# Kernel optimization log

Measured on AMD Instinct MI355X. Metric: run time of the kernel, lower is better.

The kernel has to match this reference:

```python
import jax, jax.numpy as jnp
import numpy as np

CH = 256
GROUPS = 8
EPS = 1e-5


def setup_inputs() -> dict:
    key = jax.random.key(0)
    ks = jax.random.split(key, 12)
    b, c, h, w = 8, CH, 64, 64
    s = 0.02
    return {
        "x": jax.random.normal(ks[0], (b, c, h, w), dtype=jnp.float32),
        "gn_w": jnp.ones((c,), dtype=jnp.float32),
        "gn_b": jnp.zeros((c,), dtype=jnp.float32),
        "wq": jax.random.normal(ks[1], (c, c), dtype=jnp.float32) * s,
        "bq": jax.random.normal(ks[2], (c,), dtype=jnp.float32) * s,
        "wk": jax.random.normal(ks[3], (c, c), dtype=jnp.float32) * s,
        "bk": jax.random.normal(ks[4], (c,), dtype=jnp.float32) * s,
        "wv": jax.random.normal(ks[5], (c, c), dtype=jnp.float32) * s,
        "bv": jax.random.normal(ks[6], (c,), dtype=jnp.float32) * s,
        "wp": jax.random.normal(ks[7], (c, c), dtype=jnp.float32) * s,
        "bp": jax.random.normal(ks[8], (c,), dtype=jnp.float32) * s,
    }


def reference(x, gn_w, gn_b, wq, bq, wk, bk, wv, bv, wp, bp):
    b, c, h, w = x.shape
    n = h * w
    # GroupNorm(8, c): normalize over (c//g, h, w) per group, then affine per-channel
    xg = x.reshape(b, GROUPS, c // GROUPS, n)
    mu = xg.mean(axis=(2, 3), keepdims=True)
    var = xg.var(axis=(2, 3), keepdims=True)
    y = ((xg - mu) * jax.lax.rsqrt(var + EPS)).reshape(b, c, n)
    y = y * gn_w[None, :, None] + gn_b[None, :, None]
    # 1x1 convs == channel matmuls
    q = jnp.einsum('oc,bcn->bno', wq, y) + bq              # [b, n, c]
    k = jnp.einsum('oc,bcn->bon', wk, y) + bk[:, None]     # [b, c, n]
    v = jnp.einsum('oc,bcn->bno', wv, y) + bv              # [b, n, c]
    scale = 1.0 / jnp.sqrt(jnp.float32(c))
    attn = jax.nn.softmax(jnp.einsum('bnc,bcm->bnm', q, k) * scale, axis=-1)  # [b, n, n]
    out = jnp.einsum('bnm,bmc->bcn', attn, v)              # [b, c, n]
    proj = jnp.einsum('oc,bcn->bon', wp, out) + bp[:, None]
    return x + proj.reshape(b, c, h, w)
```

## Files before the change

kernel.cpp:

```cpp
#include <hip/hip_runtime.h>

typedef __attribute__((ext_vector_type(8))) short s16x8;
typedef __attribute__((ext_vector_type(4))) float f32x4;
typedef __attribute__((ext_vector_type(16))) float f32x16;
typedef __attribute__((ext_vector_type(4))) uint u32x4;
typedef __attribute__((ext_vector_type(2))) uint u32x2;
typedef __attribute__((ext_vector_type(2))) long s64x2;
typedef __attribute__((ext_vector_type(8))) int i32x8;
typedef unsigned char u8;

#define MFMA16(a, b, c) __builtin_amdgcn_mfma_f32_16x16x32_bf16((a), (b), (c), 0, 0, 0)
#define MFMAF8(a, b, c) __builtin_amdgcn_mfma_f32_32x32x16_fp8_fp8((a), (b), (c), 0, 0, 0)
#define MFMAMX(a, b, c) \
  __builtin_amdgcn_mfma_scale_f32_32x32x64_f8f6f4((a), (b), (c), 0, 0, 0, 0x7F7F7F7F, 0, 0x7F7F7F7F)

__device__ __forceinline__ ushort f2bf(float f) {
  uint u = __builtin_bit_cast(uint, f);
  u = (u + 0x7fffu + ((u >> 16) & 1u)) >> 16;
  return (ushort)u;
}
__device__ __forceinline__ float max3f(float a, float b, float c) {
  return fmaxf(fmaxf(a, b), c);
}

__global__ __launch_bounds__(256) void cvt_w_kernel(
    const float* __restrict__ s0, const float* __restrict__ s1,
    const float* __restrict__ s2, const float* __restrict__ s3,
    ushort* __restrict__ d0, ushort* __restrict__ d1,
    ushort* __restrict__ d2, ushort* __restrict__ d3,
    const float* __restrict__ bq, const float* __restrict__ bk,
    const float* __restrict__ bv, float* __restrict__ bcat) {
  int i = blockIdx.x * 256 + threadIdx.x;
  const float4* s[4] = {(const float4*)s0, (const float4*)s1, (const float4*)s2, (const float4*)s3};
  ushort* d[4] = {d0, d1, d2, d3};
#pragma unroll
  for (int m = 0; m < 4; ++m) {
    float4 v = s[m][i];
    uint lo = (uint)f2bf(v.x) | ((uint)f2bf(v.y) << 16);
    uint hi = (uint)f2bf(v.z) | ((uint)f2bf(v.w) << 16);
    *(uint2*)(d[m] + (size_t)i * 4) = make_uint2(lo, hi);
  }
  if (blockIdx.x == 0) {
    int t = threadIdx.x;
    bcat[t] = bq[t];
    bcat[256 + t] = bk[t];
    bcat[512 + t] = bv[t];
  }
}

__global__ __launch_bounds__(256) void gn_stats_kernel(
    const float* __restrict__ x, float2* __restrict__ partial) {
  int bid = blockIdx.x;
  int b = bid >> 6, g = (bid >> 3) & 7, sl = bid & 7;
  const float4* src = (const float4*)(x + ((size_t)b * 256 + g * 32) * 4096) + sl * 4096;
  float s = 0.f, ss = 0.f;
#pragma unroll 4
  for (int i = threadIdx.x; i < 4096; i += 256) {
    float4 v = src[i];
    s += v.x + v.y + v.z + v.w;
    ss += v.x * v.x + v.y * v.y + v.z * v.z + v.w * v.w;
  }
#pragma unroll
  for (int off = 32; off; off >>= 1) {
    s += __shfl_down(s, off);
    ss += __shfl_down(ss, off);
  }
  __shared__ float ps[4], pss[4];
  int w = threadIdx.x >> 6, lane = threadIdx.x & 63;
  if (lane == 0) { ps[w] = s; pss[w] = ss; }
  __syncthreads();
  if (threadIdx.x == 0) {
    float2 r;
    r.x = ps[0] + ps[1] + ps[2] + ps[3];
    r.y = pss[0] + pss[1] + pss[2] + pss[3];
    partial[bid] = r;
  }
}

__global__ __launch_bounds__(256) void gn_apply_kernel(
    const float* __restrict__ x, const float2* __restrict__ partial,
    const float* __restrict__ gw, const float* __restrict__ gb,
    ushort* __restrict__ y) {
  int bid = blockIdx.x;
  int b = bid >> 8;
  int rem = bid & 255;
  int ct = rem >> 6, nt = rem & 63;
  int t = threadIdx.x;
  __shared__ float xs[64][65];
  __shared__ float smu2[2], srs2[2];
  if (t < 2) {
    float S = 0.f, SS = 0.f;
#pragma unroll
    for (int i = 0; i < 8; ++i) {
      float2 p = partial[(b << 6) | ((2 * ct + t) << 3) | i];
      S += p.x;
      SS += p.y;
    }
    float mu = S * (1.f / 131072.f);
    float var = SS * (1.f / 131072.f) - mu * mu;
    smu2[t] = mu;
    srs2[t] = rsqrtf(var + 1e-5f);
  }
  const float* xb = x + ((size_t)b * 256 + ct * 64) * 4096 + nt * 64;
  {
    int r = t >> 2, q = t & 3;
    const float4* src = (const float4*)(xb + (size_t)r * 4096 + q * 16);
#pragma unroll
    for (int i = 0; i < 4; ++i) {
      float4 v = src[i];
      xs[r][q * 16 + i * 4 + 0] = v.x;
      xs[r][q * 16 + i * 4 + 1] = v.y;
      xs[r][q * 16 + i * 4 + 2] = v.z;
      xs[r][q * 16 + i * 4 + 3] = v.w;
    }
  }
  __syncthreads();
  {
    int nr = t >> 2, q = t & 3;
    int c0 = q * 16;
    ushort tmp[16];
#pragma unroll
    for (int i = 0; i < 16; ++i) {
      int ci = c0 + i;
      int ch = ct * 64 + ci;
      int gsel = ci >> 5;
      float sc = gw[ch] * srs2[gsel];
      float sh = gb[ch] - smu2[gsel] * sc;
      float v = xs[ci][nr] * sc + sh;
      tmp[i] = f2bf(v);
    }
    ushort* dst = y + ((size_t)b * 4096 + nt * 64 + nr) * 256 + ct * 64 + c0;
    uint p[8];
#pragma unroll
    for (int j = 0; j < 8; ++j) p[j] = (uint)tmp[2 * j] | ((uint)tmp[2 * j + 1] << 16);
    *(uint4*)dst = make_uint4(p[0], p[1], p[2], p[3]);
    *((uint4*)dst + 1) = make_uint4(p[4], p[5], p[6], p[7]);
  }
}

template <int MODE>
__global__ __launch_bounds__(256) void gemm_bt(
    const ushort* __restrict__ A, const ushort* __restrict__ B,
    size_t aB, size_t bB, int M, int N,
    const float* __restrict__ bias, const float* __restrict__ resid,
    size_t rB, void* __restrict__ Cout, size_t cB) {
  int mTiles = M >> 7;
  int tm = blockIdx.x % mTiles, tn = blockIdx.x / mTiles;
  const ushort* Ab = A + blockIdx.y * aB + (size_t)tm * 128 * 256;
  const ushort* Bb = B + blockIdx.y * bB + (size_t)tn * 128 * 256;

  __shared__ ushort As[2][8192];
  __shared__ ushort Bs[2][8192];

  int t = threadIdx.x, lane = t & 63, w = t >> 6;
  int wr = w >> 1, wc = w & 1, lq = lane & 15, lg = lane >> 4;

  f32x4 acc[4][4];
#pragma unroll
  for (int i = 0; i < 4; ++i)
#pragma unroll
    for (int j = 0; j < 4; ++j) acc[i][j] = f32x4{0.f, 0.f, 0.f, 0.f};

  auto stageT = [&](int kb, int db) {
#pragma unroll
    for (int i = 0; i < 4; ++i) {
      int bu = i * 256 + w * 64;
      int u = bu + lane;
      int row = u >> 3, c = u & 7;
      int cl = c ^ (row & 7);
      const ushort* sa = Ab + (size_t)row * 256 + kb * 64 + cl * 8;
      __builtin_amdgcn_global_load_lds(
          (const __attribute__((address_space(1))) uint*)sa,
          (__attribute__((address_space(3))) uint*)(&As[db][0] + bu * 8), 16, 0, 0);
      const ushort* sb = Bb + (size_t)row * 256 + kb * 64 + cl * 8;
      __builtin_amdgcn_global_load_lds(
          (const __attribute__((address_space(1))) uint*)sb,
          (__attribute__((address_space(3))) uint*)(&Bs[db][0] + bu * 8), 16, 0, 0);
    }
  };

  stageT(0, 0);

#pragma unroll 1
  for (int kb = 0; kb < 4; ++kb) {
    if (kb < 3) {
      stageT(kb + 1, (kb + 1) & 1);
      asm volatile("s_waitcnt vmcnt(8)" ::: "memory");
    } else {
      asm volatile("s_waitcnt vmcnt(0)" ::: "memory");
    }
    __builtin_amdgcn_s_barrier();
    const ushort* Abf = &As[kb & 1][0];
    const ushort* Bbf = &Bs[kb & 1][0];
#pragma unroll
    for (int ks = 0; ks < 2; ++ks) {
      s16x8 af[4], bf[4];
#pragma unroll
      for (int mt = 0; mt < 4; ++mt) {
        int row = wr * 64 + mt * 16 + lq;
        af[mt] = *(const s16x8*)&Abf[row * 64 + (((ks * 4 + lg) ^ (row & 7)) << 3)];
      }
#pragma unroll
      for (int nt = 0; nt < 4; ++nt) {
        int row = wc * 64 + nt * 16 + lq;
        bf[nt] = *(const s16x8*)&Bbf[row * 64 + (((ks * 4 + lg) ^ (row & 7)) << 3)];
      }
#pragma unroll
      for (int mt = 0; mt < 4; ++mt)
#pragma unroll
        for (int nt = 0; nt < 4; ++nt)
          acc[mt][nt] = MFMA16(af[mt], bf[nt], acc[mt][nt]);
    }
    asm volatile("" ::: "memory");
    __builtin_amdgcn_s_barrier();
    asm volatile("" ::: "memory");
  }

  int mBase = tm * 128 + wr * 64;
  int nBase = tn * 128 + wc * 64;
#pragma unroll
  for (int mt = 0; mt < 4; ++mt) {
#pragma unroll
    for (int nt = 0; nt < 4; ++nt) {
#pragma unroll
      for (int r = 0; r < 4; ++r) {
        int row = mBase + mt * 16 + lg * 4 + r;
        int col = nBase + nt * 16 + lq;
        float v = acc[mt][nt][r];
        if (MODE == 6) {
          v += bias[col];
          uint pk8 = (uint)__builtin_amdgcn_cvt_pk_fp8_f32(v, v, 0, false);
          u8* Cb = (u8*)Cout + blockIdx.y * cB;
          if (col < 512) {
            u8* C = Cb + ((col >= 256) ? 16777216 : 0);
            C[(size_t)row * 256 + (col & 255)] = (u8)(pk8 & 0xff);
          } else {
            int rr = row & 31;
            int pr = (row & ~31) |
                     ((rr & 7) | (((rr >> 4) & 1) << 3) | (((rr >> 3) & 1) << 4));
            u8* C = Cb + 33554432;
            C[(size_t)(col - 512) * 4096 + pr] = (u8)(pk8 & 0xff);
          }
        } else {
          v += bias[row];
          size_t idx = (size_t)row * N + col;
          float* C = (float*)Cout + blockIdx.y * cB;
          C[idx] = v + resid[blockIdx.y * rB + idx];
        }
      }
    }
  }
}

__global__ __launch_bounds__(256, 2) void attn11_kernel(
    const u8* __restrict__ q, const u8* __restrict__ k,
    const u8* __restrict__ vT, ushort* __restrict__ pb0,
    ushort* __restrict__ pb1, float* __restrict__ mlbuf) {
  const int bb = blockIdx.x & 7;
  const int rem = blockIdx.x >> 3;
  const int qt = rem & 31;
  const int half = rem >> 5;
  const int t = threadIdx.x, w = t >> 6, lane = t & 63;
  const int lq = lane & 31, lh = lane >> 5;

  __shared__ u8 Lf[65536];

  const u8* kb = k + (size_t)bb * (4096 * 256);
  const u8* vb = vT + (size_t)bb * (4096 * 256);

  const int qrow = bb * 4096 + qt * 128 + w * 32 + lq;
  i32x8 qf8[4];
  {
    const u8* qp = q + (size_t)qrow * 256 + lh * 32;
#pragma unroll
    for (int ks = 0; ks < 4; ++ks) {
      u32x4 lo = *(const u32x4*)(qp + ks * 64);
      u32x4 hi = *(const u32x4*)(qp + ks * 64 + 16);
      qf8[ks] = i32x8{(int)lo[0], (int)lo[1], (int)lo[2], (int)lo[3],
                      (int)hi[0], (int)hi[1], (int)hi[2], (int)hi[3]};
    }
  }
  f32x16 oacc[8];
#pragma unroll
  for (int i = 0; i < 8; ++i) oacc[i] = (f32x16)(0.f);
  float mrun = -3e38f, lrun = 0.f;
  const float cs = 0.0625f * 1.44269504f;

  auto stage = [&](int it, int db) {
    const int ci = half * 64 + it;
    const u8* kcb = kb + (size_t)ci * (32 * 256);
    const u8* vcb = vb + (size_t)ci * 32;
    u8* base = Lf + db * 16384;
#pragma unroll
    for (int i = 0; i < 2; ++i) {
      int bu = w * 128 + i * 64;
      int Pu = bu + lane;
      {
        int Lu = Pu ^ ((Pu >> 4) & 7);
        const u8* ksrc = kcb + (Lu >> 4) * 256 + (Lu & 15) * 16;
        __builtin_amdgcn_global_load_lds(
            (const __attribute__((address_space(1))) uint*)ksrc,
            (__attribute__((address_space(3))) uint*)(base + bu * 16), 16, 0, 0);
      }
      {
        int Lu = Pu ^ ((Pu >> 3) & 7);
        const u8* vsrc = vcb + (size_t)(Lu >> 1) * 4096 + (Lu & 1) * 16;
        __builtin_amdgcn_global_load_lds(
            (const __attribute__((address_space(1))) uint*)vsrc,
            (__attribute__((address_space(3))) uint*)(base + 8192 + bu * 16), 16, 0, 0);
      }
    }
  };

  stage(0, 0);

#pragma unroll 1
  for (int j = 0; j < 64; ++j) {
    if (j < 63) {
      stage(j + 1, (j + 1) & 1);
      asm volatile("s_waitcnt vmcnt(4)" ::: "memory");
    } else {
      asm volatile("s_waitcnt vmcnt(0)" ::: "memory");
    }
    __builtin_amdgcn_s_barrier();

    const u8* Kbf = Lf + (j & 1) * 16384;
    const u8* Vbf = Kbf + 8192;

    __builtin_amdgcn_s_setprio(1);
    f32x16 sA = (f32x16)(0.f), sB = (f32x16)(0.f);
#pragma unroll
    for (int ks = 0; ks < 4; ++ks) {
      int u0 = (lq * 16 + ks * 4 + lh * 2) ^ (lq & 7);
      int u1 = (lq * 16 + ks * 4 + lh * 2 + 1) ^ (lq & 7);
      u32x4 k0 = *(const u32x4*)(Kbf + u0 * 16);
      u32x4 k1 = *(const u32x4*)(Kbf + u1 * 16);
      i32x8 kf = i32x8{(int)k0[0], (int)k0[1], (int)k0[2], (int)k0[3],
                       (int)k1[0], (int)k1[1], (int)k1[2], (int)k1[3]};
      if (ks & 1) sB = MFMAMX(kf, qf8[ks], sB);
      else        sA = MFMAMX(kf, qf8[ks], sA);
    }
    __builtin_amdgcn_s_setprio(0);
    float tv[16];
#pragma unroll
    for (int r = 0; r < 16; ++r) tv[r] = sA[r] + sB[r];
    float g0 = max3f(tv[0], tv[1], tv[2]);
    float g1 = max3f(tv[3], tv[4], tv[5]);
    float g2 = max3f(tv[6], tv[7], tv[8]);
    float g3 = max3f(tv[9], tv[10], tv[11]);
    float g4 = max3f(tv[12], tv[13], tv[14]);
    float pmax_t = max3f(max3f(g0, g1, tv[15]), fmaxf(g2, g3), g4);
    pmax_t = fmaxf(pmax_t, __shfl_xor(pmax_t, 32));
    float pmax = pmax_t * cs;
    if (!__all(pmax - mrun <= 8.f)) {
      float mnew = fmaxf(mrun, pmax);
      float alpha = __builtin_exp2f(mrun - mnew);
#pragma unroll
      for (int i = 0; i < 8; ++i) oacc[i] *= alpha;
      lrun *= alpha;
      mrun = mnew;
    }
    float nm = -mrun;
    float sv[16], psum = 0.f;
#pragma unroll
    for (int r = 0; r < 16; ++r) {
      sv[r] = __builtin_exp2f(__builtin_fmaf(tv[r], cs, nm));
      psum += sv[r];
    }
    psum += __shfl_xor(psum, 32);
    lrun += psum;
    uint Aw = (uint)__builtin_amdgcn_cvt_pk_fp8_f32(sv[0], sv[1], 0, false);
    Aw = (uint)__builtin_amdgcn_cvt_pk_fp8_f32(sv[2], sv[3], (int)Aw, true);
    uint Bw = (uint)__builtin_amdgcn_cvt_pk_fp8_f32(sv[4], sv[5], 0, false);
    Bw = (uint)__builtin_amdgcn_cvt_pk_fp8_f32(sv[6], sv[7], (int)Bw, true);
    uint Cw = (uint)__builtin_amdgcn_cvt_pk_fp8_f32(sv[8], sv[9], 0, false);
    Cw = (uint)__builtin_amdgcn_cvt_pk_fp8_f32(sv[10], sv[11], (int)Cw, true);
    uint Dw = (uint)__builtin_amdgcn_cvt_pk_fp8_f32(sv[12], sv[13], 0, false);
    Dw = (uint)__builtin_amdgcn_cvt_pk_fp8_f32(sv[14], sv[15], (int)Dw, true);
    asm("v_permlane32_swap_b32 %0, %1" : "+v"(Aw), "+v"(Bw));
    asm("v_permlane32_swap_b32 %0, %1" : "+v"(Cw), "+v"(Dw));
    long pf0 = __builtin_bit_cast(long, (u32x2){Aw, Bw});
    long pf1 = __builtin_bit_cast(long, (u32x2){Cw, Dw});
    __builtin_amdgcn_s_setprio(1);
#pragma unroll
    for (int db = 0; db < 8; ++db) {
      int L = (db * 32 + lq) * 2 + lh;
      int Pu = L ^ ((L >> 3) & 7);
      u32x4 vr = *(const u32x4*)(Vbf + Pu * 16);
      s64x2 vp = __builtin_bit_cast(s64x2, vr);
      oacc[db] = MFMAF8(vp[0], pf0, oacc[db]);
      oacc[db] = MFMAF8(vp[1], pf1, oacc[db]);
    }
    __builtin_amdgcn_s_setprio(0);
    asm volatile("" ::: "memory");
    __builtin_amdgcn_s_barrier();
    asm volatile("" ::: "memory");
  }

  {
    uint* wregu = (uint*)Lf + w * 4096;
#pragma unroll
    for (int db = 0; db < 8; ++db)
#pragma unroll
      for (int rp = 0; rp < 8; ++rp) {
        int r0 = rp * 2;
        int d0 = db * 32 + (r0 & 3) + 8 * (r0 >> 2) + 4 * lh;
        uint pk;
        asm("v_cvt_pk_bf16_f32 %0, %1, %2"
            : "=v"(pk) : "v"(oacc[db][r0]), "v"(oacc[db][r0 + 1]));
        int idx = lq * 128 + (d0 >> 1);
        wregu[idx ^ ((lq & 7) << 2)] = pk;
      }
    if (lh == 0) {
      int idx = half * 32768 + bb * 4096 + qt * 128 + w * 32 + lq;
      mlbuf[idx] = mrun;
      mlbuf[65536 + idx] = lrun;
    }
  }
  __syncthreads();
  {
    int r = t >> 1;
    int wv2 = r >> 5, lqr = r & 31;
    const uint* basep = (const uint*)Lf + wv2 * 4096;
    ushort* pbase = half ? pb1 : pb0;
    ushort* dstr = pbase + ((size_t)bb * 4096 + qt * 128 + r) * 256 + (t & 1) * 128;
#pragma unroll
    for (int jj = 0; jj < 16; ++jj) {
      int ui = lqr * 128 + (t & 1) * 64 + jj * 4;
      u32x4 v = *(const u32x4*)(basep + (ui ^ ((lqr & 7) << 2)));
      *(u32x4*)(dstr + jj * 8) = v;
    }
  }
}

__global__ __launch_bounds__(256) void attn_merge_kernel(
    const ushort* __restrict__ pb0, const ushort* __restrict__ pb1,
    const float* __restrict__ mlbuf, ushort* __restrict__ o) {
  int gr = blockIdx.x * 8 + (threadIdx.x >> 5);
  int dq = threadIdx.x & 31;
  float m0 = mlbuf[gr], m1 = mlbuf[32768 + gr];
  float l0 = mlbuf[65536 + gr], l1 = mlbuf[65536 + 32768 + gr];
  float M = fmaxf(m0, m1);
  float e0 = __builtin_exp2f(m0 - M), e1 = __builtin_exp2f(m1 - M);
  float inv = 1.f / (l0 * e0 + l1 * e1);
  float w0 = e0 * inv, w1 = e1 * inv;
  const size_t off = (size_t)gr * 256 + dq * 8;
  u32x4 a = *(const u32x4*)(pb0 + off);
  u32x4 b = *(const u32x4*)(pb1 + off);
  uint outw[4];
#pragma unroll
  for (int i = 0; i < 4; ++i) {
    float alo = __builtin_bit_cast(float, a[i] << 16);
    float ahi = __builtin_bit_cast(float, a[i] & 0xffff0000u);
    float blo = __builtin_bit_cast(float, b[i] << 16);
    float bhi = __builtin_bit_cast(float, b[i] & 0xffff0000u);
    float flo = alo * w0 + blo * w1;
    float fhi = ahi * w0 + bhi * w1;
    asm("v_cvt_pk_bf16_f32 %0, %1, %2" : "=v"(outw[i]) : "v"(flo), "v"(fhi));
  }
  u32x4 ov = {outw[0], outw[1], outw[2], outw[3]};
  *(u32x4*)(o + off) = ov;
}

extern "C" void kernel_launch(void* const* d_in, const int* in_sizes, int n_in,
                              void* d_out, int out_size, void* d_ws, size_t ws_size,
                              hipStream_t stream) {
  const float* x   = (const float*)d_in[0];
  const float* gnw = (const float*)d_in[1];
  const float* gnb = (const float*)d_in[2];
  const float* wq  = (const float*)d_in[3];
  const float* bq  = (const float*)d_in[4];
  const float* wk  = (const float*)d_in[5];
  const float* bk  = (const float*)d_in[6];
  const float* wv  = (const float*)d_in[7];
  const float* bv  = (const float*)d_in[8];
  const float* wp  = (const float*)d_in[9];
  const float* bp  = (const float*)d_in[10];

  const size_t SEQ = 4096, CH = 256;
  const size_t MAT = SEQ * CH;
  char* ws = (char*)d_ws;
  const size_t BUF = 8 * MAT * 2;
  ushort* y    = (ushort*)(ws + 0 * BUF);
  u8*     qb8  = (u8*)(ws + 1 * BUF);
  u8*     kb8  = (u8*)(ws + 2 * BUF);
  u8*     vtb8 = (u8*)(ws + 3 * BUF);
  ushort* pb1  = (ushort*)(ws + 4 * BUF);
  ushort* pb0  = y;
  ushort* oab  = (ushort*)(ws + 1 * BUF);
  ushort* wqb  = (ushort*)(ws + 5 * BUF);
  ushort* wkb  = wqb + 65536;
  ushort* wvb  = wkb + 65536;
  ushort* wpb  = wvb + 65536;
  float*  bcat   = (float*)(wpb + 65536);
  float2* partial = (float2*)(bcat + 768);
  float*  mlbuf  = (float*)d_out;

  cvt_w_kernel<<<64, 256, 0, stream>>>(wq, wk, wv, wp, wqb, wkb, wvb, wpb,
                                       bq, bk, bv, bcat);
  gn_stats_kernel<<<512, 256, 0, stream>>>(x, partial);
  gn_apply_kernel<<<2048, 256, 0, stream>>>(x, partial, gnw, gnb, y);

  gemm_bt<6><<<dim3(192, 8), 256, 0, stream>>>(y, wqb, MAT, 0, 4096, 768, bcat,
                                               nullptr, 0, qb8, MAT);

  attn11_kernel<<<512, 256, 0, stream>>>(qb8, kb8, vtb8, pb0, pb1, mlbuf);
  attn_merge_kernel<<<4096, 256, 0, stream>>>(pb0, pb1, mlbuf, oab);

  gemm_bt<2><<<dim3(64, 8), 256, 0, stream>>>(wpb, oab, 0, MAT, 256, 4096, bp,
                                              x, MAT, d_out, MAT);
}
```

Baseline: 199.9 us.

## Load full K=256 tiles into LDS at once instead of double-buffered K-steps

The GEMM kernel now stages the entire 128x256 A and B tiles into LDS (128 KB total) with one batch of async global-to-LDS loads, then runs all four K-blocks of MFMA with no per-step barriers. This removes the three per-iteration barrier/wait points of the double-buffered pipeline and allows full unrolling. In exchange, LDS use per block grows from 64 KB to 128 KB, which cuts occupancy to one block per CU. Load latency is also fully exposed before any compute starts.

```diff
diff --git a/kernel.cpp b/kernel.cpp
--- a/kernel.cpp
+++ b/kernel.cpp
@@ -149,8 +149,8 @@
   const ushort* Ab = A + blockIdx.y * aB + (size_t)tm * 128 * 256;
   const ushort* Bb = B + blockIdx.y * bB + (size_t)tn * 128 * 256;
 
-  __shared__ ushort As[2][8192];
-  __shared__ ushort Bs[2][8192];
+  __shared__ ushort As[32768];
+  __shared__ ushort Bs[32768];
 
   int t = threadIdx.x, lane = t & 63, w = t >> 6;
   int wr = w >> 1, wc = w & 1, lq = lane & 15, lg = lane >> 4;
@@ -161,49 +161,40 @@
 #pragma unroll
     for (int j = 0; j < 4; ++j) acc[i][j] = f32x4{0.f, 0.f, 0.f, 0.f};
 
-  auto stageT = [&](int kb, int db) {
-#pragma unroll
-    for (int i = 0; i < 4; ++i) {
-      int bu = i * 256 + w * 64;
-      int u = bu + lane;
-      int row = u >> 3, c = u & 7;
-      int cl = c ^ (row & 7);
-      const ushort* sa = Ab + (size_t)row * 256 + kb * 64 + cl * 8;
-      __builtin_amdgcn_global_load_lds(
-          (const __attribute__((address_space(1))) uint*)sa,
-          (__attribute__((address_space(3))) uint*)(&As[db][0] + bu * 8), 16, 0, 0);
-      const ushort* sb = Bb + (size_t)row * 256 + kb * 64 + cl * 8;
-      __builtin_amdgcn_global_load_lds(
-          (const __attribute__((address_space(1))) uint*)sb,
-          (__attribute__((address_space(3))) uint*)(&Bs[db][0] + bu * 8), 16, 0, 0);
-    }
-  };
-
-  stageT(0, 0);
-
-#pragma unroll 1
+#pragma unroll
+  for (int i = 0; i < 16; ++i) {
+    int bu = i * 256 + w * 64;
+    int u = bu + lane;
+    int row = u >> 5, c = u & 31;
+    int cl = (c & ~7) | ((c & 7) ^ (row & 7));
+    const ushort* sa = Ab + (size_t)row * 256 + cl * 8;
+    __builtin_amdgcn_global_load_lds(
+        (const __attribute__((address_space(1))) uint*)sa,
+        (__attribute__((address_space(3))) uint*)(As + bu * 8), 16, 0, 0);
+    const ushort* sb = Bb + (size_t)row * 256 + cl * 8;
+    __builtin_amdgcn_global_load_lds(
+        (const __attribute__((address_space(1))) uint*)sb,
+        (__attribute__((address_space(3))) uint*)(Bs + bu * 8), 16, 0, 0);
+  }
+  asm volatile("s_waitcnt vmcnt(0)" ::: "memory");
+  __builtin_amdgcn_s_barrier();
+
+#pragma unroll
   for (int kb = 0; kb < 4; ++kb) {
-    if (kb < 3) {
-      stageT(kb + 1, (kb + 1) & 1);
-      asm volatile("s_waitcnt vmcnt(8)" ::: "memory");
-    } else {
-      asm volatile("s_waitcnt vmcnt(0)" ::: "memory");
-    }
-    __builtin_amdgcn_s_barrier();
-    const ushort* Abf = &As[kb & 1][0];
-    const ushort* Bbf = &Bs[kb & 1][0];
 #pragma unroll
     for (int ks = 0; ks < 2; ++ks) {
       s16x8 af[4], bf[4];
 #pragma unroll
       for (int mt = 0; mt < 4; ++mt) {
         int row = wr * 64 + mt * 16 + lq;
-        af[mt] = *(const s16x8*)&Abf[row * 64 + (((ks * 4 + lg) ^ (row & 7)) << 3)];
+        int unit = kb * 8 + ((ks * 4 + lg) ^ (row & 7));
+        af[mt] = *(const s16x8*)&As[row * 256 + unit * 8];
       }
 #pragma unroll
       for (int nt = 0; nt < 4; ++nt) {
         int row = wc * 64 + nt * 16 + lq;
-        bf[nt] = *(const s16x8*)&Bbf[row * 64 + (((ks * 4 + lg) ^ (row & 7)) << 3)];
+        int unit = kb * 8 + ((ks * 4 + lg) ^ (row & 7));
+        bf[nt] = *(const s16x8*)&Bs[row * 256 + unit * 8];
       }
 #pragma unroll
       for (int mt = 0; mt < 4; ++mt)
@@ -211,9 +202,6 @@
         for (int nt = 0; nt < 4; ++nt)
           acc[mt][nt] = MFMA16(af[mt], bf[nt], acc[mt][nt]);
     }
-    asm volatile("" ::: "memory");
-    __builtin_amdgcn_s_barrier();
-    asm volatile("" ::: "memory");
   }
 
   int mBase = tm * 128 + wr * 64;
```

New measurement: 209.3 us. 1.05x slower.

## Fuse split-attention merge into output projection GEMM B-tile loading

Applied to the files above, without the earlier changes.

Removes the separate attention merge kernel and instead merges the two partial attention outputs, using their max/sum statistics, while loading B tiles in a new dedicated projection GEMM. This avoids writing and rereading the merged bf16 attention output and saves one kernel launch. In exchange the GEMM loads two partial buffers per tile, recomputes the merge weights redundantly across the tiles that share rows, and uses a register-staged B path instead of direct-to-LDS loads. The mlbuf scratch space moves from the output buffer into the workspace.

```diff
diff --git a/kernel.cpp b/kernel.cpp
--- a/kernel.cpp
+++ b/kernel.cpp
@@ -252,6 +252,142 @@
   }
 }
 
+__global__ __launch_bounds__(256) void gemm_proj_kernel(
+    const ushort* __restrict__ A, const ushort* __restrict__ P0,
+    const ushort* __restrict__ P1, const float* __restrict__ mlb,
+    const float* __restrict__ bias, const float* __restrict__ resid,
+    float* __restrict__ Cout) {
+  const size_t MAT = 4096 * 256;
+  int tm = blockIdx.x & 1, tn = blockIdx.x >> 1;
+  int bb = blockIdx.y;
+  const ushort* Ab = A + (size_t)tm * 128 * 256;
+  const ushort* P0b = P0 + (size_t)bb * MAT + (size_t)tn * 128 * 256;
+  const ushort* P1b = P1 + (size_t)bb * MAT + (size_t)tn * 128 * 256;
+  const int mlbase = bb * 4096 + tn * 128;
+
+  __shared__ ushort As[2][8192];
+  __shared__ ushort Bs[2][8192];
+
+  int t = threadIdx.x, lane = t & 63, w = t >> 6;
+  int wr = w >> 1, wc = w & 1, lq = lane & 15, lg = lane >> 4;
+
+  f32x4 acc[4][4];
+#pragma unroll
+  for (int i = 0; i < 4; ++i)
+#pragma unroll
+    for (int j = 0; j < 4; ++j) acc[i][j] = f32x4{0.f, 0.f, 0.f, 0.f};
+
+  u32x4 rb0[4], rb1[4];
+  float rw0[4], rw1[4];
+
+  auto issueA = [&](int kb, int db) {
+#pragma unroll
+    for (int i = 0; i < 4; ++i) {
+      int bu = i * 256 + w * 64;
+      int u = bu + lane;
+      int row = u >> 3, c = u & 7;
+      int cl = c ^ (row & 7);
+      const ushort* sa = Ab + (size_t)row * 256 + kb * 64 + cl * 8;
+      __builtin_amdgcn_global_load_lds(
+          (const __attribute__((address_space(1))) uint*)sa,
+          (__attribute__((address_space(3))) uint*)(&As[db][0] + bu * 8), 16, 0, 0);
+    }
+  };
+  auto loadB = [&](int kb) {
+#pragma unroll
+    for (int i = 0; i < 4; ++i) {
+      int bu = i * 256 + w * 64;
+      int u = bu + lane;
+      int row = u >> 3, c = u & 7;
+      int cl = c ^ (row & 7);
+      rb0[i] = *(const u32x4*)(P0b + (size_t)row * 256 + kb * 64 + cl * 8);
+      rb1[i] = *(const u32x4*)(P1b + (size_t)row * 256 + kb * 64 + cl * 8);
+      int gr = mlbase + row;
+      float m0 = mlb[gr], m1 = mlb[32768 + gr];
+      float l0 = mlb[65536 + gr], l1 = mlb[98304 + gr];
+      float M = fmaxf(m0, m1);
+      float e0 = __builtin_exp2f(m0 - M), e1 = __builtin_exp2f(m1 - M);
+      float inv = 1.f / (l0 * e0 + l1 * e1);
+      rw0[i] = e0 * inv;
+      rw1[i] = e1 * inv;
+    }
+  };
+  auto writeB = [&](int db) {
+#pragma unroll
+    for (int i = 0; i < 4; ++i) {
+      int bu = i * 256 + w * 64;
+      uint outw[4];
+#pragma unroll
+      for (int j = 0; j < 4; ++j) {
+        float alo = __builtin_bit_cast(float, rb0[i][j] << 16);
+        float ahi = __builtin_bit_cast(float, rb0[i][j] & 0xffff0000u);
+        float blo = __builtin_bit_cast(float, rb1[i][j] << 16);
+        float bhi = __builtin_bit_cast(float, rb1[i][j] & 0xffff0000u);
+        float flo = alo * rw0[i] + blo * rw1[i];
+        float fhi = ahi * rw0[i] + bhi * rw1[i];
+        asm("v_cvt_pk_bf16_f32 %0, %1, %2" : "=v"(outw[j]) : "v"(flo), "v"(fhi));
+      }
+      u32x4 ov = {outw[0], outw[1], outw[2], outw[3]};
+      *(u32x4*)&Bs[db][(size_t)(bu + lane) * 8] = ov;
+    }
+  };
+
+  issueA(0, 0);
+  loadB(0);
+  writeB(0);
+  asm volatile("s_waitcnt vmcnt(0) lgkmcnt(0)" ::: "memory");
+  __builtin_amdgcn_s_barrier();
+
+#pragma unroll
+  for (int kb = 0; kb < 4; ++kb) {
+    const int db = kb & 1;
+    if (kb < 3) {
+      issueA(kb + 1, db ^ 1);
+      loadB(kb + 1);
+    }
+    const ushort* Abf = &As[db][0];
+    const ushort* Bbf = &Bs[db][0];
+#pragma unroll
+    for (int ks = 0; ks < 2; ++ks) {
+      s16x8 af[4], bf[4];
+#pragma unroll
+      for (int mt = 0; mt < 4; ++mt) {
+        int row = wr * 64 + mt * 16 + lq;
+        af[mt] = *(const s16x8*)&Abf[row * 64 + (((ks * 4 + lg) ^ (row & 7)) << 3)];
+      }
+#pragma unroll
+      for (int nt = 0; nt < 4; ++nt) {
+        int row = wc * 64 + nt * 16 + lq;
+        bf[nt] = *(const s16x8*)&Bbf[row * 64 + (((ks * 4 + lg) ^ (row & 7)) << 3)];
+      }
+#pragma unroll
+      for (int mt = 0; mt < 4; ++mt)
+#pragma unroll
+        for (int nt = 0; nt < 4; ++nt)
+          acc[mt][nt] = MFMA16(af[mt], bf[nt], acc[mt][nt]);
+    }
+    if (kb < 3) writeB(db ^ 1);
+    asm volatile("s_waitcnt vmcnt(0) lgkmcnt(0)" ::: "memory");
+    __builtin_amdgcn_s_barrier();
+  }
+
+  int mBase = tm * 128 + wr * 64;
+  int nBase = tn * 128 + wc * 64;
+#pragma unroll
+  for (int mt = 0; mt < 4; ++mt) {
+#pragma unroll
+    for (int nt = 0; nt < 4; ++nt) {
+#pragma unroll
+      for (int r = 0; r < 4; ++r) {
+        int row = mBase + mt * 16 + lg * 4 + r;
+        int col = nBase + nt * 16 + lq;
+        size_t idx = (size_t)bb * MAT + (size_t)row * 4096 + col;
+        Cout[idx] = acc[mt][nt][r] + bias[row] + resid[idx];
+      }
+    }
+  }
+}
+
 __global__ __launch_bounds__(256, 2) void attn11_kernel(
     const u8* __restrict__ q, const u8* __restrict__ k,
     const u8* __restrict__ vT, ushort* __restrict__ pb0,
@@ -433,35 +569,6 @@
   }
 }
 
-__global__ __launch_bounds__(256) void attn_merge_kernel(
-    const ushort* __restrict__ pb0, const ushort* __restrict__ pb1,
-    const float* __restrict__ mlbuf, ushort* __restrict__ o) {
-  int gr = blockIdx.x * 8 + (threadIdx.x >> 5);
-  int dq = threadIdx.x & 31;
-  float m0 = mlbuf[gr], m1 = mlbuf[32768 + gr];
-  float l0 = mlbuf[65536 + gr], l1 = mlbuf[65536 + 32768 + gr];
-  float M = fmaxf(m0, m1);
-  float e0 = __builtin_exp2f(m0 - M), e1 = __builtin_exp2f(m1 - M);
-  float inv = 1.f / (l0 * e0 + l1 * e1);
-  float w0 = e0 * inv, w1 = e1 * inv;
-  const size_t off = (size_t)gr * 256 + dq * 8;
-  u32x4 a = *(const u32x4*)(pb0 + off);
-  u32x4 b = *(const u32x4*)(pb1 + off);
-  uint outw[4];
-#pragma unroll
-  for (int i = 0; i < 4; ++i) {
-    float alo = __builtin_bit_cast(float, a[i] << 16);
-    float ahi = __builtin_bit_cast(float, a[i] & 0xffff0000u);
-    float blo = __builtin_bit_cast(float, b[i] << 16);
-    float bhi = __builtin_bit_cast(float, b[i] & 0xffff0000u);
-    float flo = alo * w0 + blo * w1;
-    float fhi = ahi * w0 + bhi * w1;
-    asm("v_cvt_pk_bf16_f32 %0, %1, %2" : "=v"(outw[i]) : "v"(flo), "v"(fhi));
-  }
-  u32x4 ov = {outw[0], outw[1], outw[2], outw[3]};
-  *(u32x4*)(o + off) = ov;
-}
-
 extern "C" void kernel_launch(void* const* d_in, const int* in_sizes, int n_in,
                               void* d_out, int out_size, void* d_ws, size_t ws_size,
                               hipStream_t stream) {
@@ -487,14 +594,13 @@
   u8*     vtb8 = (u8*)(ws + 3 * BUF);
   ushort* pb1  = (ushort*)(ws + 4 * BUF);
   ushort* pb0  = y;
-  ushort* oab  = (ushort*)(ws + 1 * BUF);
   ushort* wqb  = (ushort*)(ws + 5 * BUF);
   ushort* wkb  = wqb + 65536;
   ushort* wvb  = wkb + 65536;
   ushort* wpb  = wvb + 65536;
   float*  bcat   = (float*)(wpb + 65536);
   float2* partial = (float2*)(bcat + 768);
-  float*  mlbuf  = (float*)d_out;
+  float*  mlbuf  = (float*)(partial + 512);
 
   cvt_w_kernel<<<64, 256, 0, stream>>>(wq, wk, wv, wp, wqb, wkb, wvb, wpb,
                                        bq, bk, bv, bcat);
@@ -505,8 +611,7 @@
                                                nullptr, 0, qb8, MAT);
 
   attn11_kernel<<<512, 256, 0, stream>>>(qb8, kb8, vtb8, pb0, pb1, mlbuf);
-  attn_merge_kernel<<<4096, 256, 0, stream>>>(pb0, pb1, mlbuf, oab);
-
-  gemm_bt<2><<<dim3(64, 8), 256, 0, stream>>>(wpb, oab, 0, MAT, 256, 4096, bp,
-                                              x, MAT, d_out, MAT);
-}
+
+  gemm_proj_kernel<<<dim3(64, 8), 256, 0, stream>>>(wpb, pb0, pb1, mlbuf, bp,
+                                                    x, (float*)d_out);
+}
```

After: 196.3 us. No clear change (-1.8%).
